# Kernel optimization log

Hardware: AMD Instinct MI355X
Metric: run time of the kernel (lower is better)

## Reference

```python
import jax, jax.numpy as jnp
import numpy as np

B, N, D = 16, 1024, 5
R_HID = 8  # radial MLP hidden width


def setup_inputs() -> dict:
    key = jax.random.key(0)
    ks = jax.random.split(key, 16)
    feats = jax.random.normal(ks[0], (B, N, D), jnp.float32)
    coors = 3.0 * jax.random.normal(ks[1], (B, N, 3), jnp.float32)
    a = jax.random.bernoulli(ks[2], 0.01, (B, N, N))
    adj_mat = a | jnp.swapaxes(a, 1, 2)
    s = 1.0 / np.sqrt(D)
    Wq = s * jax.random.normal(ks[3], (D, D), jnp.float32)
    Wk = s * jax.random.normal(ks[4], (D, D), jnp.float32)
    Wv = s * jax.random.normal(ks[5], (D, D), jnp.float32)
    Wo = s * jax.random.normal(ks[6], (D, D), jnp.float32)
    w_r1 = 0.5 * jax.random.normal(ks[7], (1, R_HID), jnp.float32)
    b_r1 = jnp.zeros((R_HID,), jnp.float32)
    w_r2 = 0.5 * jax.random.normal(ks[8], (R_HID, 1), jnp.float32)
    b_r2 = jnp.zeros((1,), jnp.float32)
    w1 = (1.0 / np.sqrt(D)) * jax.random.normal(ks[9], (D, 128), jnp.float32)
    b1 = jnp.zeros((128,), jnp.float32)
    w2 = (1.0 / np.sqrt(128.0)) * jax.random.normal(ks[10], (128, 3), jnp.float32)
    b2 = jnp.zeros((3,), jnp.float32)
    return dict(feats=feats, coors=coors, adj_mat=adj_mat, Wq=Wq, Wk=Wk, Wv=Wv,
                Wo=Wo, w_r1=w_r1, b_r1=b_r1, w_r2=w_r2, b_r2=b_r2,
                w1=w1, b1=b1, w2=w2, b2=b2)


def _se3_layer(feats, coors, neigh, Wq, Wk, Wv, Wo, w_r1, b_r1, w_r2, b_r2):
    # SE(3)-invariant sparse graph attention on degree-0 channels.
    # Attention logits = content term + radial (distance-only) bias, so the
    # scalar output is invariant to global rotations/translations of coors.
    q = jnp.einsum('bnd,de->bne', feats, Wq)
    k = jnp.einsum('bnd,de->bne', feats, Wk)
    v = jnp.einsum('bnd,de->bne', feats, Wv)
    rel = coors[:, :, None, :] - coors[:, None, :, :]        # [B,N,N,3]
    dist = jnp.sqrt(jnp.sum(rel * rel, axis=-1) + 1e-8)      # [B,N,N]
    h = jax.nn.relu(dist[..., None] * w_r1[0] + b_r1)        # [B,N,N,R_HID]
    rbias = (h @ w_r2)[..., 0] + b_r2[0]                     # [B,N,N]
    scores = jnp.einsum('bid,bjd->bij', q, k) / np.sqrt(q.shape[-1]) + rbias
    scores = jnp.where(neigh, scores, -1e9)
    attn = jax.nn.softmax(scores, axis=-1)
    agg = jnp.einsum('bij,bjd->bid', attn, v)
    return feats + jnp.einsum('bid,de->bie', agg, Wo)        # residual


def reference(feats, coors, adj_mat, Wq, Wk, Wv, Wo, w_r1, b_r1, w_r2, b_r2,
              w1, b1, w2, b2):
    a = adj_mat.astype(jnp.float32)
    # num_adj_degrees=2: attend over 1-hop and 2-hop neighbors (+ self)
    adj2 = jnp.einsum('bij,bjk->bik', a, a) > 0
    eye = jnp.eye(adj_mat.shape[1], dtype=bool)[None]
    neigh = adj_mat | adj2 | eye
    x = _se3_layer(feats, coors, neigh, Wq, Wk, Wv, Wo, w_r1, b_r1, w_r2, b_r2)
    pooled = jnp.mean(x, axis=1)                              # [B, D]
    hdn = jax.nn.relu(pooled @ w1 + b1)
    return hdn @ w2 + b2                                      # [B, 3]
```

## Files before the change

### kernel.cpp

```cpp
#include <hip/hip_runtime.h>
#include <hip/hip_bf16.h>

#define BB 16
#define NN 1024
#define DD 5
#define RH 8

typedef unsigned long long u64;
typedef unsigned int u32;
typedef __hip_bfloat16 bf16;

static __device__ __forceinline__ float tof(bf16 x) { return __bfloat162float(x); }
static __device__ __forceinline__ float ldf(const void* p, long long i, bool f) {
  return f ? ((const float*)p)[i] : tof(((const bf16*)p)[i]);
}

#define LOG2E 1.4426950408889634f
#define PACK_BLOCKS (BB * NN * 16 / 256)
#define KV_BLOCKS (BB * NN / 256)


__global__ __launch_bounds__(256) void k_pack(
    const void* __restrict__ adj, const void* __restrict__ feats,
    const void* __restrict__ coors,
    const void* __restrict__ Wk, const void* __restrict__ Wv,
    const void* __restrict__ Wo,
    u64* __restrict__ adjbits, float4* __restrict__ kvg,
    float* __restrict__ czg, int* __restrict__ gflags,
    float* __restrict__ pooled, int* __restrict__ cntr) {
  __shared__ int sNon01, sNonpair, sLow3;
  __shared__ int sCnt[4];
  __shared__ float wkL[25], wvL[25], woL[25];
  int tid = threadIdx.x;

  if (blockIdx.x >= PACK_BLOCKS) {
    int kb = blockIdx.x - PACK_BLOCKS;
    if (kb == 0) {
      if (tid < BB * DD) pooled[tid] = 0.0f;
      else if (tid < BB * DD + BB) cntr[tid - BB * DD] = 0;
    }
    {
      u32 x = ((const u32*)feats)[tid];
      u32 lo = x & 0xFFFFu;
      int e = (int)((lo >> 7) & 0xFFu);
      bool insane = !(lo == 0u || (e >= 90 && e <= 150));
      u64 m = __ballot(insane);
      if ((tid & 63) == 0) sCnt[tid >> 6] = (int)__popcll(m);
    }
    __syncthreads();
    bool f32 = (sCnt[0] + sCnt[1] + sCnt[2] + sCnt[3]) > 64;
    if (tid < 25) {
      wkL[tid] = ldf(Wk, tid, f32);
      wvL[tid] = ldf(Wv, tid, f32);
      woL[tid] = ldf(Wo, tid, f32);
    }
    if (kb == 0 && tid == 0) gflags[0] = f32 ? 1 : 0;
    __syncthreads();
    long long node = (long long)kb * 256 + tid;
    float f0 = ldf(feats, node * DD + 0, f32), f1 = ldf(feats, node * DD + 1, f32),
          f2 = ldf(feats, node * DD + 2, f32), f3 = ldf(feats, node * DD + 3, f32),
          f4 = ldf(feats, node * DD + 4, f32);
    float k[DD], tv[DD], v[DD];
    #pragma unroll
    for (int e = 0; e < DD; ++e) {
      k[e] = f0 * wkL[e] + f1 * wkL[5 + e] + f2 * wkL[10 + e] + f3 * wkL[15 + e] +
             f4 * wkL[20 + e];
      tv[e] = f0 * wvL[e] + f1 * wvL[5 + e] + f2 * wvL[10 + e] + f3 * wvL[15 + e] +
              f4 * wvL[20 + e];
    }
    #pragma unroll
    for (int e = 0; e < DD; ++e)
      v[e] = tv[0] * woL[e] + tv[1] * woL[5 + e] + tv[2] * woL[10 + e] +
             tv[3] * woL[15 + e] + tv[4] * woL[20 + e];
    float cx = ldf(coors, node * 3 + 0, f32);
    float cy = ldf(coors, node * 3 + 1, f32);
    float cz = ldf(coors, node * 3 + 2, f32);
    kvg[node * 3 + 0] = make_float4(k[0], k[1], k[2], k[3]);
    kvg[node * 3 + 1] = make_float4(k[4], v[0], v[1], v[2]);
    kvg[node * 3 + 2] = make_float4(v[3], v[4], cx, cy);
    czg[node] = cz;
    return;
  }

  if (tid == 0) { sNon01 = 0; sNonpair = 0; sLow3 = 0; }
  __syncthreads();
  {
    const u32* aw = (const u32*)adj;
    int non01 = 0, nonpair = 0, low3 = 0;
    for (int i = tid; i < 4096; i += 256) {
      u32 x = aw[i];
      u32 lo = x & 0xFFFFu, hi = x >> 16;
      non01 |= (x > 1u);
      nonpair |= !((lo == 0u || lo == 0x3F80u) && (hi == 0u || hi == 0x3F80u));
      low3 |= (lo == 0x3F80u);
    }
    if (non01) atomicOr(&sNon01, 1);
    if (nonpair) atomicOr(&sNonpair, 1);
    if (low3) atomicOr(&sLow3, 1);
  }
  __syncthreads();
  int mode;
  if (!sNon01) mode = 0;
  else if (!sNonpair) mode = sLow3 ? 2 : 3;
  else mode = 1;

  int gid = blockIdx.x * 256 + tid;
  int w = gid & 15;
  long long row = gid >> 4;
  long long base = row * NN + (long long)w * 64;
  u64 bits = 0;
  if (mode == 3) {
    const uint4* p = (const uint4*)((const float*)adj + base);
    #pragma unroll
    for (int t = 0; t < 16; ++t) {
      uint4 x = p[t];
      if (x.x << 1) bits |= 1ull << (4 * t + 0);
      if (x.y << 1) bits |= 1ull << (4 * t + 1);
      if (x.z << 1) bits |= 1ull << (4 * t + 2);
      if (x.w << 1) bits |= 1ull << (4 * t + 3);
    }
  } else if (mode == 0) {
    const uint4* p = (const uint4*)((const u32*)adj + base);
    #pragma unroll
    for (int t = 0; t < 16; ++t) {
      uint4 x = p[t];
      if (x.x) bits |= 1ull << (4 * t + 0);
      if (x.y) bits |= 1ull << (4 * t + 1);
      if (x.z) bits |= 1ull << (4 * t + 2);
      if (x.w) bits |= 1ull << (4 * t + 3);
    }
  } else if (mode == 2) {
    const uint4* p = (const uint4*)((const unsigned short*)adj + base);
    #pragma unroll
    for (int t = 0; t < 8; ++t) {
      uint4 x = p[t];
      u32 c[4] = {x.x, x.y, x.z, x.w};
      #pragma unroll
      for (int q = 0; q < 4; ++q) {
        if ((c[q] & 0x7FFFu)) bits |= 1ull << (8 * t + 2 * q + 0);
        if ((c[q] >> 16) & 0x7FFFu) bits |= 1ull << (8 * t + 2 * q + 1);
      }
    }
  } else {
    const uint4* p = (const uint4*)((const unsigned char*)adj + base);
    #pragma unroll
    for (int t = 0; t < 4; ++t) {
      uint4 x = p[t];
      u32 c[4] = {x.x, x.y, x.z, x.w};
      #pragma unroll
      for (int q = 0; q < 4; ++q)
        #pragma unroll
        for (int bb = 0; bb < 4; ++bb)
          if ((c[q] >> (8 * bb)) & 0xFFu) bits |= 1ull << (16 * t + 4 * q + bb);
    }
  }
  adjbits[gid] = bits;
}

__global__ __launch_bounds__(256) void k_attn(
    const void* __restrict__ feats, const void* __restrict__ coors,
    const void* __restrict__ Wq,
    const void* __restrict__ wr1, const void* __restrict__ br1,
    const void* __restrict__ wr2, const void* __restrict__ br2,
    const float4* __restrict__ kvg, const float* __restrict__ czg,
    const int* __restrict__ gflags, const u64* __restrict__ adjbits,
    float* __restrict__ pooled, int* __restrict__ cntr,
    const void* __restrict__ w1, const void* __restrict__ b1,
    const void* __restrict__ w2, const void* __restrict__ b2,
    float* __restrict__ out) {
  __shared__ __align__(16) float4 kvT[2][3][64];
  __shared__ float czT[2][64];
  __shared__ unsigned short listL[4][NN];
  __shared__ u64 neighL[16][16];
  __shared__ float qL[16 * DD], ciL[16 * 3];
  __shared__ float wqL[25];
  __shared__ float wrL[3][RH];
  __shared__ float sConst[2];
  __shared__ int sFast, sLast;
  __shared__ float waveC[4][DD];
  __shared__ float pM[DD];
  __shared__ float hL[128];

  int bi = blockIdx.x;
  int b = bi >> 6, chunk = bi & 63;
  int tid = threadIdx.x;

  const float4* kvb3 = kvg + (size_t)b * NN * 3;
  const float* czb = czg + (size_t)b * NN;
  float4 stg;
  float stgc;
  if (tid < 192) stg = kvb3[tid];
  else stgc = czb[tid - 192];

  bool f32 = gflags[0] != 0;
  if (tid < 25) wqL[tid] = ldf(Wq, tid, f32);
  if (tid >= 64 && tid < 64 + RH) {
    int h = tid - 64;
    wrL[0][h] = ldf(wr1, h, f32);
    wrL[1][h] = ldf(br1, h, f32);
    wrL[2][h] = ldf(wr2, h, f32);
  }
  if (tid == 96) {
    float c = 0.0f;
    int ok = 1;
    #pragma unroll
    for (int h = 0; h < RH; ++h) {
      float w1h = ldf(wr1, h, f32);
      if (ldf(br1, h, f32) != 0.0f) ok = 0;
      if (w1h > 0.0f) c += w1h * ldf(wr2, h, f32);
    }
    sConst[0] = c * LOG2E;
    sConst[1] = ldf(br2, 0, f32) * LOG2E;
    sFast = ok;
  }
  __syncthreads();
  int fast = sFast;
  if (tid < 16) {
    long long row = (long long)b * NN + chunk * 16 + tid;
    float f0 = ldf(feats, row * DD + 0, f32), f1 = ldf(feats, row * DD + 1, f32),
          f2 = ldf(feats, row * DD + 2, f32), f3 = ldf(feats, row * DD + 3, f32),
          f4 = ldf(feats, row * DD + 4, f32);
    float qsc = fast ? (0.4472135954999579f * LOG2E) : 0.4472135954999579f;
    #pragma unroll
    for (int e = 0; e < DD; ++e)
      qL[tid * DD + e] = (f0 * wqL[e] + f1 * wqL[5 + e] + f2 * wqL[10 + e] +
                          f3 * wqL[15 + e] + f4 * wqL[20 + e]) * qsc;
    #pragma unroll
    for (int c = 0; c < 3; ++c)
      ciL[tid * 3 + c] = ldf(coors, row * 3 + c, f32);
  }

  int g = tid >> 6, lane = tid & 63;
  int w = lane & 15, grp = lane >> 4;
  const u64* basep = adjbits + (size_t)b * NN * 16;
  for (int rr = 0; rr < 4; ++rr) {
    int il = g * 4 + rr;
    int i = chunk * 16 + il;
    u64 rw = basep[(size_t)i * 16 + w];
    unsigned short* list = listL[g];
    int cnt = 0;
    #pragma unroll
    for (int sw = 0; sw < 16; ++sw) {
      u64 bits = __shfl(rw, sw, 64);
      int mybit = (int)((bits >> lane) & 1ull);
      int pre = __popcll(bits & ((1ull << lane) - 1ull));
      if (mybit) list[cnt + pre] = (unsigned short)(sw * 64 + lane);
      cnt += __popcll(bits);
    }
    u64 acc = rw;
    if (w == (i >> 6)) acc |= 1ull << (i & 63);
    for (int n = grp; n < cnt; n += 4) acc |= basep[(size_t)list[n] * 16 + w];
    acc |= __shfl_xor(acc, 16, 64);
    acc |= __shfl_xor(acc, 32, 64);
    if (lane < 16) neighL[il][lane] = acc;
  }

  if (tid < 192) kvT[0][tid % 3][tid / 3] = stg;
  else czT[0][tid - 192] = stgc;
  __syncthreads();

  float q[4][DD], ci[4][3], l[4], A[4][DD];
  #pragma unroll
  for (int r = 0; r < 4; ++r) {
    #pragma unroll
    for (int e = 0; e < DD; ++e) q[r][e] = qL[(g * 4 + r) * DD + e];
    #pragma unroll
    for (int c = 0; c < 3; ++c) ci[r][c] = ciL[(g * 4 + r) * 3 + c];
    l[r] = 0.0f;
    #pragma unroll
    for (int e = 0; e < DD; ++e) A[r][e] = 0.0f;
  }
  float Cf = sConst[0], br2f = sConst[1];
  int cur = 0;
  for (int t = 0; t < 16; ++t) {
    if (t < 15) {
      if (tid < 192) stg = kvb3[(size_t)(t + 1) * 192 + tid];
      else stgc = czb[(t + 1) * 64 + (tid - 192)];
    }
    float4 ka = kvT[cur][0][lane];
    float4 kb = kvT[cur][1][lane];
    float4 kc = kvT[cur][2][lane];
    float jz = czT[cur][lane];
    float jx = kc.z, jy = kc.w;
    u64 nw[4];
    #pragma unroll
    for (int r = 0; r < 4; ++r) nw[r] = neighL[g * 4 + r][t];
    if (fast) {
      #pragma unroll
      for (int r = 0; r < 4; ++r) {
        float cx = jx - ci[r][0], cy = jy - ci[r][1], cz = jz - ci[r][2];
        float dist =
            __builtin_amdgcn_sqrtf(fmaf(cx, cx, fmaf(cy, cy, fmaf(cz, cz, 1e-8f))));
        float s = fmaf(q[r][0], ka.x, br2f);
        s = fmaf(q[r][1], ka.y, s);
        s = fmaf(q[r][2], ka.z, s);
        s = fmaf(q[r][3], ka.w, s);
        s = fmaf(q[r][4], kb.x, s);
        s = fmaf(Cf, dist, s);
        s = fminf(s, 126.0f);
        s = ((nw[r] >> lane) & 1ull) ? s : -150.0f;
        float p = __builtin_amdgcn_exp2f(s);
        l[r] += p;
        A[r][0] = fmaf(p, kb.y, A[r][0]);
        A[r][1] = fmaf(p, kb.z, A[r][1]);
        A[r][2] = fmaf(p, kb.w, A[r][2]);
        A[r][3] = fmaf(p, kc.x, A[r][3]);
        A[r][4] = fmaf(p, kc.y, A[r][4]);
      }
    } else {
      #pragma unroll
      for (int r = 0; r < 4; ++r) {
        float cx = jx - ci[r][0], cy = jy - ci[r][1], cz = jz - ci[r][2];
        float dist = sqrtf(fmaf(cx, cx, fmaf(cy, cy, fmaf(cz, cz, 1e-8f))));
        float rb = ldf(br2, 0, f32);
        #pragma unroll
        for (int h = 0; h < RH; ++h)
          rb += fmaxf(dist * wrL[0][h] + wrL[1][h], 0.0f) * wrL[2][h];
        float s = fmaf(q[r][0], ka.x, rb);
        s = fmaf(q[r][1], ka.y, s);
        s = fmaf(q[r][2], ka.z, s);
        s = fmaf(q[r][3], ka.w, s);
        s = fmaf(q[r][4], kb.x, s);
        s = fminf(s, 85.0f);
        s = ((nw[r] >> lane) & 1ull) ? s : -100.0f;
        float p = __expf(s);
        l[r] += p;
        A[r][0] = fmaf(p, kb.y, A[r][0]);
        A[r][1] = fmaf(p, kb.z, A[r][1]);
        A[r][2] = fmaf(p, kb.w, A[r][2]);
        A[r][3] = fmaf(p, kc.x, A[r][3]);
        A[r][4] = fmaf(p, kc.y, A[r][4]);
      }
    }
    if (t < 15) {
      if (tid < 192) kvT[cur ^ 1][tid % 3][tid / 3] = stg;
      else czT[cur ^ 1][tid - 192] = stgc;
    }
    __syncthreads();
    cur ^= 1;
  }
  #pragma unroll
  for (int msk = 1; msk < 64; msk <<= 1) {
    #pragma unroll
    for (int r = 0; r < 4; ++r) {
      l[r] += __shfl_xor(l[r], msk, 64);
      A[r][0] += __shfl_xor(A[r][0], msk, 64);
      A[r][1] += __shfl_xor(A[r][1], msk, 64);
      A[r][2] += __shfl_xor(A[r][2], msk, 64);
      A[r][3] += __shfl_xor(A[r][3], msk, 64);
      A[r][4] += __shfl_xor(A[r][4], msk, 64);
    }
  }

  if (lane == 0) {
    float cw[DD] = {0.f, 0.f, 0.f, 0.f, 0.f};
    #pragma unroll
    for (int r = 0; r < 4; ++r) {
      long long grow = (long long)b * NN + chunk * 16 + g * 4 + r;
      float inv = (l[r] > 0.0f) ? 1.0f / l[r] : 0.0f;
      #pragma unroll
      for (int e = 0; e < DD; ++e)
        cw[e] += ldf(feats, grow * DD + e, f32) + A[r][e] * inv;
    }
    #pragma unroll
    for (int e = 0; e < DD; ++e) waveC[g][e] = cw[e];
  }
  __syncthreads();
  if (tid < DD) {
    float s = waveC[0][tid] + waveC[1][tid] + waveC[2][tid] + waveC[3][tid];
    float old = atomicAdd(&pooled[b * DD + tid], s);
    asm volatile("" :: "v"(old));
  }
  __syncthreads();
  if (tid == 0) sLast = (atomicAdd(&cntr[b], 1) == 63) ? 1 : 0;
  __syncthreads();

  if (sLast) {
    if (tid < DD) {
      float pv = __hip_atomic_load(&pooled[b * DD + tid], __ATOMIC_RELAXED,
                                   __HIP_MEMORY_SCOPE_AGENT);
      pM[tid] = pv * (1.0f / 1024.0f);
    }
    __syncthreads();
    if (tid < 128) {
      float acc = ldf(b1, tid, f32);
      #pragma unroll
      for (int d = 0; d < DD; ++d)
        acc = fmaf(pM[d], ldf(w1, d * 128 + tid, f32), acc);
      hL[tid] = fmaxf(acc, 0.0f);
    }
    __syncthreads();
    if (tid < 3) {
      float s = ldf(b2, tid, f32);
      for (int j2 = 0; j2 < 128; ++j2)
        s = fmaf(hL[j2], ldf(w2, j2 * 3 + tid, f32), s);
      out[b * 3 + tid] = s;
    }
  }
}

extern "C" void kernel_launch(void* const* d_in, const int* in_sizes, int n_in,
                              void* d_out, int out_size, void* d_ws, size_t ws_size,
                              hipStream_t stream) {
  const void* adj = d_in[2];
  float* out = (float*)d_out;

  char* w = (char*)d_ws;
  int* gflags = (int*)w;
  float* pooled = (float*)(w + 64);
  int* cntr = (int*)(w + 512);
  const size_t MB2 = (size_t)BB * NN * 16 * sizeof(u64);
  u64* adjbits = (u64*)(w + 1024);
  float4* kvg = (float4*)(w + 1024 + MB2);
  float* czg = (float*)(w + 1024 + MB2 + 786432);

  k_pack<<<PACK_BLOCKS + KV_BLOCKS, 256, 0, stream>>>(
      adj, d_in[0], d_in[1], d_in[4], d_in[5], d_in[6], adjbits, kvg, czg,
      gflags, pooled, cntr);
  k_attn<<<BB * 64, 256, 0, stream>>>(
      d_in[0], d_in[1], d_in[3], d_in[7], d_in[8], d_in[9], d_in[10], kvg, czg,
      gflags, adjbits, pooled, cntr, d_in[11], d_in[12], d_in[13], d_in[14],
      out);
}
```

Measured before the change: 190.2 us.

## Split attention key range across two blocks per row chunk with atomic merge

```diff
diff --git a/kernel.cpp b/kernel.cpp
--- a/kernel.cpp
+++ b/kernel.cpp
@@ -27,7 +27,8 @@
     const void* __restrict__ Wo,
     u64* __restrict__ adjbits, float4* __restrict__ kvg,
     float* __restrict__ czg, int* __restrict__ gflags,
-    float* __restrict__ pooled, int* __restrict__ cntr) {
+    float* __restrict__ pooled, int* __restrict__ cntr,
+    int* __restrict__ cnt2, float* __restrict__ rowAgg) {
   __shared__ int sNon01, sNonpair, sLow3;
   __shared__ int sCnt[4];
   __shared__ float wkL[25], wvL[25], woL[25];
@@ -38,6 +39,7 @@
     if (kb == 0) {
       if (tid < BB * DD) pooled[tid] = 0.0f;
       else if (tid < BB * DD + BB) cntr[tid - BB * DD] = 0;
+      for (int i = tid; i < BB * 64; i += 256) cnt2[i] = 0;
     }
     {
       u32 x = ((const u32*)feats)[tid];
@@ -57,6 +59,8 @@
     if (kb == 0 && tid == 0) gflags[0] = f32 ? 1 : 0;
     __syncthreads();
     long long node = (long long)kb * 256 + tid;
+    #pragma unroll
+    for (int c = 0; c < 6; ++c) rowAgg[node * 6 + c] = 0.0f;
     float f0 = ldf(feats, node * DD + 0, f32), f1 = ldf(feats, node * DD + 1, f32),
           f2 = ldf(feats, node * DD + 2, f32), f3 = ldf(feats, node * DD + 3, f32),
           f4 = ldf(feats, node * DD + 4, f32);
@@ -164,32 +168,36 @@
     const void* __restrict__ wr2, const void* __restrict__ br2,
     const float4* __restrict__ kvg, const float* __restrict__ czg,
     const int* __restrict__ gflags, const u64* __restrict__ adjbits,
+    float* __restrict__ rowAgg, int* __restrict__ cnt2,
     float* __restrict__ pooled, int* __restrict__ cntr,
     const void* __restrict__ w1, const void* __restrict__ b1,
     const void* __restrict__ w2, const void* __restrict__ b2,
     float* __restrict__ out) {
   __shared__ __align__(16) float4 kvT[2][3][64];
   __shared__ float czT[2][64];
-  __shared__ unsigned short listL[4][NN];
-  __shared__ u64 neighL[16][16];
+  __shared__ unsigned short listL[4][2][NN];
+  __shared__ u64 neighL[16][8];
   __shared__ float qL[16 * DD], ciL[16 * 3];
   __shared__ float wqL[25];
   __shared__ float wrL[3][RH];
   __shared__ float sConst[2];
-  __shared__ int sFast, sLast;
-  __shared__ float waveC[4][DD];
+  __shared__ int sFast, sSecond, sLast;
+  __shared__ float waveC[16][6];
+  __shared__ float finC[16][DD];
   __shared__ float pM[DD];
   __shared__ float hL[128];
 
   int bi = blockIdx.x;
-  int b = bi >> 6, chunk = bi & 63;
+  int b = bi >> 7, rem = bi & 127, chunk = rem >> 1, half = rem & 1;
   int tid = threadIdx.x;
 
-  const float4* kvb3 = kvg + (size_t)b * NN * 3;
-  const float* czb = czg + (size_t)b * NN;
+  const float4* kvb3 = kvg + ((size_t)(b * NN) + half * 512) * 3;
+  const float* czb = czg + (size_t)(b * NN) + half * 512;
+  bool ldkv = tid < 192;
+  int plane = tid >> 6, slot = tid & 63;
   float4 stg;
   float stgc;
-  if (tid < 192) stg = kvb3[tid];
+  if (ldkv) stg = kvb3[slot * 3 + plane];
   else stgc = czb[tid - 192];
 
   bool f32 = gflags[0] != 0;
@@ -231,13 +239,15 @@
   }
 
   int g = tid >> 6, lane = tid & 63;
-  int w = lane & 15, grp = lane >> 4;
+  int w16 = lane & 15;
+  int wc = lane & 7, grp8 = lane >> 3;
+  int hc = half * 8 + wc;
   const u64* basep = adjbits + (size_t)b * NN * 16;
   for (int rr = 0; rr < 4; ++rr) {
     int il = g * 4 + rr;
     int i = chunk * 16 + il;
-    u64 rw = basep[(size_t)i * 16 + w];
-    unsigned short* list = listL[g];
+    u64 rw = basep[(size_t)i * 16 + w16];
+    unsigned short* list = listL[g][rr & 1];
     int cnt = 0;
     #pragma unroll
     for (int sw = 0; sw < 16; ++sw) {
@@ -247,15 +257,17 @@
       if (mybit) list[cnt + pre] = (unsigned short)(sw * 64 + lane);
       cnt += __popcll(bits);
     }
-    u64 acc = rw;
-    if (w == (i >> 6)) acc |= 1ull << (i & 63);
-    for (int n = grp; n < cnt; n += 4) acc |= basep[(size_t)list[n] * 16 + w];
+    u64 acc = __shfl(rw, hc, 64);
+    if (hc == (i >> 6)) acc |= 1ull << (i & 63);
+    for (int n = grp8; n < cnt; n += 8)
+      acc |= basep[(size_t)list[n] * 16 + hc];
+    acc |= __shfl_xor(acc, 8, 64);
     acc |= __shfl_xor(acc, 16, 64);
     acc |= __shfl_xor(acc, 32, 64);
-    if (lane < 16) neighL[il][lane] = acc;
-  }
-
-  if (tid < 192) kvT[0][tid % 3][tid / 3] = stg;
+    if (lane < 8) neighL[il][lane] = acc;
+  }
+
+  if (ldkv) kvT[0][plane][slot] = stg;
   else czT[0][tid - 192] = stgc;
   __syncthreads();
 
@@ -272,9 +284,9 @@
   }
   float Cf = sConst[0], br2f = sConst[1];
   int cur = 0;
-  for (int t = 0; t < 16; ++t) {
-    if (t < 15) {
-      if (tid < 192) stg = kvb3[(size_t)(t + 1) * 192 + tid];
+  for (int t = 0; t < 8; ++t) {
+    if (t < 7) {
+      if (ldkv) stg = kvb3[(size_t)((t + 1) * 64 + slot) * 3 + plane];
       else stgc = czb[(t + 1) * 64 + (tid - 192)];
     }
     float4 ka = kvT[cur][0][lane];
@@ -332,8 +344,8 @@
         A[r][4] = fmaf(p, kc.y, A[r][4]);
       }
     }
-    if (t < 15) {
-      if (tid < 192) kvT[cur ^ 1][tid % 3][tid / 3] = stg;
+    if (t < 7) {
+      if (ldkv) kvT[cur ^ 1][plane][slot] = stg;
       else czT[cur ^ 1][tid - 192] = stgc;
     }
     __syncthreads();
@@ -353,48 +365,70 @@
   }
 
   if (lane == 0) {
-    float cw[DD] = {0.f, 0.f, 0.f, 0.f, 0.f};
     #pragma unroll
     for (int r = 0; r < 4; ++r) {
-      long long grow = (long long)b * NN + chunk * 16 + g * 4 + r;
-      float inv = (l[r] > 0.0f) ? 1.0f / l[r] : 0.0f;
-      #pragma unroll
-      for (int e = 0; e < DD; ++e)
-        cw[e] += ldf(feats, grow * DD + e, f32) + A[r][e] * inv;
-    }
-    #pragma unroll
-    for (int e = 0; e < DD; ++e) waveC[g][e] = cw[e];
-  }
-  __syncthreads();
-  if (tid < DD) {
-    float s = waveC[0][tid] + waveC[1][tid] + waveC[2][tid] + waveC[3][tid];
-    float old = atomicAdd(&pooled[b * DD + tid], s);
+      waveC[g * 4 + r][0] = l[r];
+      #pragma unroll
+      for (int e = 0; e < DD; ++e) waveC[g * 4 + r][1 + e] = A[r][e];
+    }
+  }
+  __syncthreads();
+  if (tid < 96) {
+    int rl = tid / 6, c = tid % 6;
+    float old = atomicAdd(
+        &rowAgg[((size_t)(b * NN) + chunk * 16 + rl) * 6 + c], waveC[rl][c]);
     asm volatile("" :: "v"(old));
   }
   __syncthreads();
-  if (tid == 0) sLast = (atomicAdd(&cntr[b], 1) == 63) ? 1 : 0;
-  __syncthreads();
-
-  if (sLast) {
+  if (tid == 0) sSecond = (atomicAdd(&cnt2[(b << 6) | chunk], 1) == 1) ? 1 : 0;
+  __syncthreads();
+
+  if (sSecond) {
+    if (tid < 16) {
+      size_t row = (size_t)(b * NN) + chunk * 16 + tid;
+      float lt = __hip_atomic_load(&rowAgg[row * 6 + 0], __ATOMIC_RELAXED,
+                                   __HIP_MEMORY_SCOPE_AGENT);
+      float inv = (lt > 0.f) ? 1.0f / lt : 0.0f;
+      #pragma unroll
+      for (int e = 0; e < DD; ++e) {
+        float Ae = __hip_atomic_load(&rowAgg[row * 6 + 1 + e], __ATOMIC_RELAXED,
+                                     __HIP_MEMORY_SCOPE_AGENT);
+        finC[tid][e] = ldf(feats, (long long)row * DD + e, f32) + Ae * inv;
+      }
+    }
+    __syncthreads();
     if (tid < DD) {
-      float pv = __hip_atomic_load(&pooled[b * DD + tid], __ATOMIC_RELAXED,
-                                   __HIP_MEMORY_SCOPE_AGENT);
-      pM[tid] = pv * (1.0f / 1024.0f);
-    }
-    __syncthreads();
-    if (tid < 128) {
-      float acc = ldf(b1, tid, f32);
-      #pragma unroll
-      for (int d = 0; d < DD; ++d)
-        acc = fmaf(pM[d], ldf(w1, d * 128 + tid, f32), acc);
-      hL[tid] = fmaxf(acc, 0.0f);
-    }
-    __syncthreads();
-    if (tid < 3) {
-      float s = ldf(b2, tid, f32);
-      for (int j2 = 0; j2 < 128; ++j2)
-        s = fmaf(hL[j2], ldf(w2, j2 * 3 + tid, f32), s);
-      out[b * 3 + tid] = s;
+      float s = 0.0f;
+      #pragma unroll
+      for (int k = 0; k < 16; ++k) s += finC[k][tid];
+      float old = atomicAdd(&pooled[b * DD + tid], s);
+      asm volatile("" :: "v"(old));
+    }
+    __syncthreads();
+    if (tid == 0) sLast = (atomicAdd(&cntr[b], 1) == 63) ? 1 : 0;
+    __syncthreads();
+
+    if (sLast) {
+      if (tid < DD) {
+        float pv = __hip_atomic_load(&pooled[b * DD + tid], __ATOMIC_RELAXED,
+                                     __HIP_MEMORY_SCOPE_AGENT);
+        pM[tid] = pv * (1.0f / 1024.0f);
+      }
+      __syncthreads();
+      if (tid < 128) {
+        float acc = ldf(b1, tid, f32);
+        #pragma unroll
+        for (int d = 0; d < DD; ++d)
+          acc = fmaf(pM[d], ldf(w1, d * 128 + tid, f32), acc);
+        hL[tid] = fmaxf(acc, 0.0f);
+      }
+      __syncthreads();
+      if (tid < 3) {
+        float s = ldf(b2, tid, f32);
+        for (int j2 = 0; j2 < 128; ++j2)
+          s = fmaf(hL[j2], ldf(w2, j2 * 3 + tid, f32), s);
+        out[b * 3 + tid] = s;
+      }
     }
   }
 }
@@ -409,16 +443,17 @@
   int* gflags = (int*)w;
   float* pooled = (float*)(w + 64);
   int* cntr = (int*)(w + 512);
-  const size_t MB2 = (size_t)BB * NN * 16 * sizeof(u64);
-  u64* adjbits = (u64*)(w + 1024);
-  float4* kvg = (float4*)(w + 1024 + MB2);
-  float* czg = (float*)(w + 1024 + MB2 + 786432);
+  int* cnt2 = (int*)(w + 1024);
+  u64* adjbits = (u64*)(w + 8192);
+  float4* kvg = (float4*)(w + 2105344);
+  float* czg = (float*)(w + 2891776);
+  float* rowAgg = (float*)(w + 2957312);
 
   k_pack<<<PACK_BLOCKS + KV_BLOCKS, 256, 0, stream>>>(
       adj, d_in[0], d_in[1], d_in[4], d_in[5], d_in[6], adjbits, kvg, czg,
-      gflags, pooled, cntr);
-  k_attn<<<BB * 64, 256, 0, stream>>>(
+      gflags, pooled, cntr, cnt2, rowAgg);
+  k_attn<<<BB * 128, 256, 0, stream>>>(
       d_in[0], d_in[1], d_in[3], d_in[7], d_in[8], d_in[9], d_in[10], kvg, czg,
-      gflags, adjbits, pooled, cntr, d_in[11], d_in[12], d_in[13], d_in[14],
-      out);
+      gflags, adjbits, rowAgg, cnt2, pooled, cntr, d_in[11], d_in[12],
+      d_in[13], d_in[14], out);
 }
```

New measurement: 204.5 us. 7.5% more time.
